# Kernel optimization log

Hardware: AMD Instinct MI355X
Metric: run time of the kernel (lower is better)

The kernel has to match this reference:

```python
import jax, jax.numpy as jnp
import numpy as np

MAX_LEVEL = 3
FULL_LEN = 2 ** MAX_LEVEL  # wavelet_full_len for db1, mode='zero'


def _make_patterns():
    # Per-feature input to the DWT is [v, 0, ..., 0] (scalar zero-padded to 2**j).
    # Haar/db1 'zero' DWT of that signal is v times a fixed sparse pattern:
    # cA (len 1) = v*2^(-j/2); cD_k first element = v*2^(-k/2), rest zeros.
    pats = []
    for j in range(1, MAX_LEVEL + 1):
        vec = [2.0 ** (-j / 2.0)]                      # cA, length 1
        for k in range(1, j + 1):                      # cD_1 .. cD_j
            seg = np.zeros(2 ** (j - k))
            seg[0] = 2.0 ** (-k / 2.0)
            vec.extend(seg.tolist())
        full = np.zeros(FULL_LEN, dtype=np.float32)
        arr = np.asarray(vec, dtype=np.float32)
        full[: arr.shape[0]] = arr                     # F.pad to wavelet_full_len
        pats.append(full)
    return jnp.asarray(np.stack(pats))                 # (MAX_LEVEL, FULL_LEN)

_P = _make_patterns()


def _gumbel_hard(logits, gumb):
    # F.gumbel_softmax(logits, tau=1.0, hard=True), one sample per feature row.
    y = jax.nn.softmax(logits[None, :] + gumb, axis=-1)          # (feat, L)
    hard = jax.nn.one_hot(jnp.argmax(y, axis=-1), y.shape[-1], dtype=y.dtype)
    return jax.lax.stop_gradient(hard - y) + y                   # straight-through


def _wavelet_layer(x, logits, gumb, Wnl, bnl, Wwo, bwo):
    # Collapses the per-feature/per-level torch double loop:
    # xi_wave(level j) = v * (Wnl[f] . P[j]) + bnl[f]
    a = Wnl @ _P.T                       # (feat, levels)
    w = _gumbel_hard(logits, gumb)       # (feat, levels), one-hot rows
    coeff = jnp.sum(w * a, axis=-1)      # (feat,)
    agg = x * coeff + bnl                # (B, N, feat)
    return agg @ Wwo + bwo               # linear_out


def _mix(h, res_proj):
    diff = jnp.mean((h - res_proj) ** 2)
    th = jax.nn.sigmoid(diff)
    return th * h + (1.0 - th) * res_proj


def reference(x, adj, Wres, bres,
              Wg0, bg0, Wrg0, brg0, logits0, gumb0, Wnl0, bnl0, Wwo0, bwo0, Wrw0, brw0,
              Wg1, bg1, Wrg1, brg1, logits1, gumb1, Wnl1, bnl1, Wwo1, bwo1, Wrw1, brw1):
    res = x @ Wres + bres                                        # (B,N,Dout)
    # ---- layer 0 ----
    xg = jnp.einsum('ij,bjf->bif', adj, x) @ Wg0 + bg0           # 64->256: no residual add
    xg = _mix(xg, res @ Wrg0 + brg0)
    xw = _wavelet_layer(xg, logits0, gumb0, Wnl0, bnl0, Wwo0, bwo0) + xg  # 256==256: add
    xw = _mix(xw, res @ Wrw0 + brw0)
    # ---- layer 1 ----
    xg1 = jnp.einsum('ij,bjf->bif', adj, xw) @ Wg1 + bg1 + xw    # 256==256: add
    xg1 = _mix(xg1, res @ Wrg1 + brg1)
    xw1 = _wavelet_layer(xg1, logits1, gumb1, Wnl1, bnl1, Wwo1, bwo1)     # 256->64: no add
    xw1 = _mix(xw1, res @ Wrw1 + brw1)
    return xw1


def setup_inputs() -> dict:
    key = jax.random.key(0)
    ks = jax.random.split(key, 32)
    B, N, D_in, H, D_out = 128, 512, 64, 256, 64
    s = 0.05
    inp = {
        'x': jax.random.normal(ks[0], (B, N, D_in), jnp.float32),
        'adj': jax.random.uniform(ks[1], (N, N), jnp.float32) / N,
        'Wres': jax.random.normal(ks[2], (D_in, D_out), jnp.float32) * s,
        'bres': jax.random.normal(ks[3], (D_out,), jnp.float32) * s,
        'Wg0': jax.random.normal(ks[4], (D_in, H), jnp.float32) * s,
        'bg0': jax.random.normal(ks[5], (H,), jnp.float32) * s,
        'Wrg0': jax.random.normal(ks[6], (D_out, H), jnp.float32) * s,
        'brg0': jax.random.normal(ks[7], (H,), jnp.float32) * s,
        'logits0': jax.random.normal(ks[8], (3,), jnp.float32),
        'gumb0': jax.random.gumbel(ks[9], (H, 3), jnp.float32),
        'Wnl0': jax.random.normal(ks[10], (H, FULL_LEN), jnp.float32) * s,
        'bnl0': jax.random.normal(ks[11], (H,), jnp.float32) * s,
        'Wwo0': jax.random.normal(ks[12], (H, H), jnp.float32) * s,
        'bwo0': jax.random.normal(ks[13], (H,), jnp.float32) * s,
        'Wrw0': jax.random.normal(ks[14], (D_out, H), jnp.float32) * s,
        'brw0': jax.random.normal(ks[15], (H,), jnp.float32) * s,
        'Wg1': jax.random.normal(ks[16], (H, H), jnp.float32) * s,
        'bg1': jax.random.normal(ks[17], (H,), jnp.float32) * s,
        'Wrg1': jax.random.normal(ks[18], (D_out, H), jnp.float32) * s,
        'brg1': jax.random.normal(ks[19], (H,), jnp.float32) * s,
        'logits1': jax.random.normal(ks[20], (3,), jnp.float32),
        'gumb1': jax.random.gumbel(ks[21], (H, 3), jnp.float32),
        'Wnl1': jax.random.normal(ks[22], (H, FULL_LEN), jnp.float32) * s,
        'bnl1': jax.random.normal(ks[23], (H,), jnp.float32) * s,
        'Wwo1': jax.random.normal(ks[24], (H, D_out), jnp.float32) * s,
        'bwo1': jax.random.normal(ks[25], (D_out,), jnp.float32) * s,
        'Wrw1': jax.random.normal(ks[26], (D_out, D_out), jnp.float32) * s,
        'brw1': jax.random.normal(ks[27], (D_out,), jnp.float32) * s,
    }
    return inp
```

## Files before the change

kernel.cpp:

```cpp
#include <hip/hip_runtime.h>
#include <hip/hip_bf16.h>
#include <math.h>

#define BB   128
#define NN   512
#define DIN  64
#define HH   256
#define DOUT 64
#define BNR  (BB * NN)

typedef float  f32x4  __attribute__((ext_vector_type(4)));
typedef __bf16 bf16x8 __attribute__((ext_vector_type(8)));

#define GLP(p)  ((const __attribute__((address_space(1))) void*)(p))
#define LDSP(p) ((__attribute__((address_space(3))) void*)(p))

__constant__ float PAT[3][8] = {
    {0.70710678f, 0.70710678f, 0.f, 0.f, 0.f, 0.f, 0.f, 0.f},
    {0.5f,        0.70710678f, 0.f, 0.5f, 0.f, 0.f, 0.f, 0.f},
    {0.35355339f, 0.70710678f, 0.f, 0.f, 0.f, 0.5f, 0.f, 0.35355339f}
};

__device__ __forceinline__ unsigned short f2bfu(float x) {
    __hip_bfloat16 b = __float2bfloat16(x);
// ... 57 lines not shown
    for (int p = 0; p < BM / RPP; ++p) {
        int row = p * RPP + tid / TPR;
        int cb = (tid % TPR) * 16;
        int pb = cb ^ (((row >> 2) & 3) << 5);
        uint4 v = *reinterpret_cast<const uint4*>(lds + row * (BN * 2) + pb);
        *reinterpret_cast<uint4*>(reinterpret_cast<char*>(C + base + (long)row * N) + cb) = v;
    }
}

template<int BM, int BN, int FM, int FN>
__device__ __forceinline__ void write_tileT(char* lds, f32x4 (&a)[FM][FN],
                                            __hip_bfloat16* __restrict__ CT,
                                            long baseT, int ldT, int tid)
{
    const int wave = tid >> 6;
    const int lane = tid & 63;
    const int wm = wave >> 1, wn = wave & 1;
    const int lc = lane & 15;
    const int lr4 = (lane >> 4) << 2;
    __syncthreads();
    #pragma unroll
    for (int j = 0; j < FN; ++j) {
        int c = wn * (FN * 16) + j * 16 + lc;
        int cbase = c * (BM * 2);
        int swz = ((c >> 2) & 3) << 5;
        #pragma unroll
        for (int i = 0; i < FM; ++i) {
            int m0 = wm * (FM * 16) + i * 16 + lr4;
            #pragma unroll
            for (int r = 0; r < 4; ++r) {
                int m = m0 + r;
                *reinterpret_cast<unsigned short*>(lds + cbase + ((m * 2) ^ swz)) =
                    f2bfu(a[i][j][r]);
            }
        }
    }
    __syncthreads();
    const int TPR = BM / 8;
    const int RPP = 256 / TPR;
    #pragma unroll
    for (int p = 0; p < BN / RPP; ++p) {
        int c = p * RPP + tid / TPR;
        int tb = (tid % TPR) * 16;
        int pb = tb ^ (((c >> 2) & 3) << 5);
        uint4 v = *reinterpret_cast<const uint4*>(lds + c * (BM * 2) + pb);
        *reinterpret_cast<uint4*>(reinterpret_cast<char*>(CT + baseT + (long)c * ldT) + tb) = v;
    }
}

template<int BM, int BN>
__device__ __forceinline__ void stage_tiles(const __hip_bfloat16* __restrict__ Ab,
                                            const __hip_bfloat16* __restrict__ Bb,
                                            char* AsB, char* BsB,
                                            int m0, int n0, int k0, int KA, int KB,
                                            int wave, int lane)
{
    const int NCH = (BM + BN) / 32;
    const int lr = lane >> 3;
    const int ls = lane & 7;
    #pragma unroll
    for (int cc = 0; cc < NCH; ++cc) {
        int c = wave * NCH + cc;
        const __hip_bfloat16* src;
        char* ldsb;
        if (c < BM / 8) {
            int r = c * 8 + lr;
            ldsb = AsB + c * 1024;
            src = Ab + ((long)(m0 + r) * KA + k0 + ((ls ^ (r & 7)) << 3));
        } else {
            int c2 = c - BM / 8;
            int r = c2 * 8 + lr;
            ldsb = BsB + c2 * 1024;
            src = Bb + ((long)(n0 + r) * KB + k0 + ((ls ^ (r & 7)) << 3));
        }
        __builtin_amdgcn_global_load_lds(GLP(src), LDSP(ldsb), 16, 0, 0);
    }
}

template<int BM, int BN, int FM, int FN>
__device__ __forceinline__ void mfma_tiles(char* AsB, char* BsB,
                                           f32x4 (&acc)[FM][FN], int wave, int lane)
{
    const int wm = wave >> 1, wn = wave & 1;
    #pragma unroll
    for (int ksl = 0; ksl < 2; ++ksl) {
        bf16x8 af[FM], bfr[FN];
        #pragma unroll
        for (int i = 0; i < FM; ++i) {
            int row = wm * (FM * 16) + i * 16 + (lane & 15);
            int off = (ksl * 64 + ((lane >> 4) << 4)) ^ ((row & 7) << 4);
            af[i] = *reinterpret_cast<const bf16x8*>(AsB + row * 128 + off);
        }
        #pragma unroll
        for (int j = 0; j < FN; ++j) {
            int row = wn * (FN * 16) + j * 16 + (lane & 15);
            int off = (ksl * 64 + ((lane >> 4) << 4)) ^ ((row & 7) << 4);
            bfr[j] = *reinterpret_cast<const bf16x8*>(BsB + row * 128 + off);
        }
        #pragma unroll
        for (int i = 0; i < FM; ++i)
            #pragma unroll
            for (int j = 0; j < FN; ++j)
                acc[i][j] = __builtin_amdgcn_mfma_f32_16x16x32_bf16(
                    af[i], bfr[j], acc[i][j], 0, 0, 0);
    }
}

template<int BM, int BN, int FM, int FN, int NS, int NA>
__device__ __forceinline__ void pipe_run(
    const __hip_bfloat16* const (&sA)[NS], const __hip_bfloat16* const (&sB)[NS],
    const int (&sK)[NS], const int (&sk0)[NS],
    char* buf0, char* buf1,
    f32x4 (&acc0)[FM][FN], f32x4 (&acc1)[FM][FN],
    int m0, int n0, int wave, int lane)
{
    constexpr int BOFF = BM * 128;
    stage_tiles<BM, BN>(sA[0], sB[0], buf0, buf0 + BOFF, m0, n0, sk0[0],
                        sK[0], sK[0], wave, lane);
    __syncthreads();
    #pragma unroll
    for (int t = 0; t < NS; ++t) {
        char* bc = (t & 1) ? buf1 : buf0;
        if (t + 1 < NS) {
            char* bn = (t & 1) ? buf0 : buf1;
            stage_tiles<BM, BN>(sA[t + 1], sB[t + 1], bn, bn + BOFF, m0, n0,
                                sk0[t + 1], sK[t + 1], sK[t + 1], wave, lane);
        }
        if (t < NA) mfma_tiles<BM, BN, FM, FN>(bc, bc + BOFF, acc0, wave, lane);
        else        mfma_tiles<BM, BN, FM, FN>(bc, bc + BOFF, acc1, wave, lane);
        __syncthreads();
    }
}

__device__ __forceinline__ void tcvt_body(const float* __restrict__ in,
                                          unsigned short* __restrict__ out,
                                          const float* cs, float us,
                                          int R, int C, int r0, int c0)
{
    __shared__ float t[64][65];
    int tr = threadIdx.x >> 6;
    int tc = threadIdx.x & 63;
    #pragma unroll
    for (int i = 0; i < 16; ++i) {
        int r = i * 4 + tr;
        t[r][tc] = in[(long)(r0 + r) * C + c0 + tc];
    }
    __syncthreads();
    float sc = (cs ? cs[r0 + tc] : 1.0f) * us;
    #pragma unroll
    for (int i = 0; i < 16; ++i) {
        int r = i * 4 + tr;
        out[(long)(c0 + r) * R + r0 + tc] = f2bfu(t[tc][r] * sc);
    }
}

__device__ __forceinline__ void coeff_local(const float* lg, const float* gb,
                                            const float* Wn, float* cof, int t)
{
    float l0 = lg[0] + gb[t * 3 + 0];
    float l1 = lg[1] + gb[t * 3 + 1];
    float l2 = lg[2] + gb[t * 3 + 2];
    int bl = 0;
    float bv = l0;
    if (l1 > bv) { bv = l1; bl = 1; }
    if (l2 > bv) { bv = l2; bl = 2; }
    float s = 0.f;
    #pragma unroll
    for (int q = 0; q < 8; ++q) s += Wn[t * 8 + q] * PAT[bl][q];
    cof[t] = s;
}

struct WTArgs {
    const float* src[8];
    unsigned short* dst[8];
    int ci[8];
    float sgn[8];
    int R[8], C[8];
};
struct WFArgs {
    const float* Wsrc[4];
    const float* Wbig[4];
    int ci[4], incl[4], N[4];
    unsigned short* dst[4];
};
struct FVArgs {
    const float* W[6];
    int ci[6];
    const float* v[6];
    const float* base[6];
    float* out[6];
    int K[6], N[6];
};
struct PrepArgs {
    const float *logits0, *gumb0, *Wnl0, *logits1, *gumb1, *Wnl1;
    const float* adj;
    unsigned int* adjb;
    float* ars;
    const float* x;
    unsigned short *xbf, *xT;
};

__global__ __launch_bounds__(256) void prep_k(PrepArgs p, WTArgs wa, WFArgs wf, FVArgs fv)
{
    __shared__ float cofA[256];
    __shared__ float cofB[256];
    __shared__ float redu[256];
    const int b = blockIdx.x;
    const int t = threadIdx.x;
    if (b < NN) {
        float2 v = reinterpret_cast<const float2*>(p.adj)[b * 256 + t];
        p.adjb[b * 256 + t] = (unsigned int)f2bfu(v.x) | ((unsigned int)f2bfu(v.y) << 16);
        redu[t] = v.x + v.y;
        __syncthreads();
        for (int o = 128; o > 0; o >>= 1) {
            if (t < o) redu[t] += redu[t + o];
            __syncthreads();
        }
        if (t == 0) p.ars[b] = redu[0];
    } else if (b < NN + 8 * BB) {
        __shared__ float tl[64][65];
        int tt = b - NN;
        int bz = tt >> 3;
        int r0 = (tt & 7) * 64;
        const long base = (long)bz * NN * DIN;
        const int tr4 = t >> 6;
        const int tc  = t & 63;
        #pragma unroll
        for (int i = 0; i < 16; ++i) {
            int r = i * 4 + tr4;
            float v = p.x[base + (long)(r0 + r) * DIN + tc];
            tl[r][tc] = v;
            p.xbf[base + (long)(r0 + r) * DIN + tc] = f2bfu(v);
        }
        __syncthreads();
        #pragma unroll
        for (int i = 0; i < 16; ++i) {
            int d = i * 4 + tr4;
            p.xT[base + (long)d * NN + r0 + tc] = f2bfu(tl[tc][d]);
        }
    } else if (b < NN + 8 * BB + 128) {
        int xg = b - NN - 8 * BB;
        int wgt = xg >> 4;
        int tl2 = xg & 15;
        int R = wa.R[wgt], C = wa.C[wgt];
        int tilesX = C >> 6;
        int tiles = (R >> 6) * tilesX;
        if (tl2 >= tiles) return;
        const float* cs = nullptr;
        if (wa.ci[wgt]) {
            if (wa.ci[wgt] == 1) coeff_local(p.logits0, p.gumb0, p.Wnl0, cofA, t);
            else                 coeff_local(p.logits1, p.gumb1, p.Wnl1, cofA, t);
            __syncthreads();
            cs = cofA;
        }
        tcvt_body(wa.src[wgt], wa.dst[wgt], cs, wa.sgn[wgt], R, C,
                  (tl2 / tilesX) * 64, (tl2 % tilesX) * 64);
    } else if (b < NN + 8 * BB + 128 + 256) {
        int xg = b - NN - 8 * BB - 128;
        int cs = xg >> 6;
        int m = xg & 63;
        float cv = 1.0f;
        if (wf.ci[cs]) {
            if (wf.ci[cs] == 1) coeff_local(p.logits0, p.gumb0, p.Wnl0, cofA, t);
            else                coeff_local(p.logits1, p.gumb1, p.Wnl1, cofA, t);
            __syncthreads();
            cv = cofA[t];
        }
        cofB[t] = wf.Wsrc[cs][m * 256 + t] * cv;
        __syncthreads();
        int n = t;
        int N = wf.N[cs];
        if (n >= N) return;
        float s = wf.incl[cs] ? wf.Wsrc[cs][m * 256 + n] : 0.f;
        const float* Wb = wf.Wbig[cs];
        #pragma unroll 8
        for (int k = 0; k < 256; ++k)
            s += cofB[k] * Wb[(long)k * N + n];
        wf.dst[cs][n * 64 + m] = f2bfu(s);
    } else {
        int n = b - (NN + 8 * BB + 128 + 256);
        coeff_local(p.logits0, p.gumb0, p.Wnl0, cofA, t);
        coeff_local(p.logits1, p.gumb1, p.Wnl1, cofB, t);
        __syncthreads();
        for (int cs = 0; cs < 6; ++cs) {
            __syncthreads();
            if (n >= fv.N[cs]) continue;
            float s = 0.f;
            if (t < fv.K[cs]) {
                float cc = (fv.ci[cs] == 1) ? cofA[t] : (fv.ci[cs] == 2 ? cofB[t] : 1.0f);
                s = fv.v[cs][t] * cc * fv.W[cs][(long)t * fv.N[cs] + n];
            }
            redu[t] = s;
            __syncthreads();
            for (int o = 128; o > 0; o >>= 1) {
                if (t < o) redu[t] += redu[t + o];
                __syncthreads();
            }
            if (t == 0)
                fv.out[cs][n] = (fv.base[cs] ? fv.base[cs][n] : 0.f) + redu[0];
        }
    }
}

__global__ __launch_bounds__(256) void sc0_k(
    const float* __restrict__ partial, int np, float inv_n,
    unsigned short* __restrict__ Wa, unsigned short* __restrict__ Wb,
    const float* __restrict__ bg0p, const float* __restrict__ brg0p,
    const float* __restrict__ crow0, float* __restrict__ cv0)
{
    __shared__ float red[256];
    float th = block_th(partial, np, inv_n, red, threadIdx.x);
    float om = 1.f - th;
    int g = blockIdx.x * 256 + threadIdx.x;
    Wa[g] = f2bfu(th * bf2f(Wa[g]));
    Wb[g] = f2bfu(om * bf2f(Wb[g]));
    if (g < 256) cv0[g] = th * bg0p[g] + om * brg0p[g] + crow0[g];
}

__global__ __launch_bounds__(256) void sc1_k(
    const float* __restrict__ partial, int np, float inv_n,
    unsigned short* __restrict__ Wg1T,
    const unsigned short* __restrict__ Wrw0T, const unsigned short* __restrict__ Wrg0pT,
    unsigned short* __restrict__ WcombT,
    unsigned short* __restrict__ Wg0pT,
    unsigned short* __restrict__ WrwWg1T,
    const float* __restrict__ bg1, const float* __restrict__ brw0,
    const float* __restrict__ cv0, const float* __restrict__ bw1v,
    float* __restrict__ bv1g, float* __restrict__ bw1s)
{
    __shared__ float red[256];
    float th = block_th(partial, np, inv_n, red, threadIdx.x);
    float om = 1.f - th;
    int g = blockIdx.x * 256 + threadIdx.x;
    Wg1T[g] = f2bfu(th * bf2f(Wg1T[g]));
    if (g < 16384) {
        WcombT[g]  = f2bfu(th * bf2f(Wrg0pT[g]) + om * bf2f(Wrw0T[g]));
        Wg0pT[g]   = f2bfu(th * bf2f(Wg0pT[g]));
        WrwWg1T[g] = f2bfu(om * bf2f(WrwWg1T[g]));
    }
    if (g < 256) {
        bv1g[g] = bg1[g] + om * brw0[g] + th * cv0[g];
        bw1s[g] = om * bw1v[g];
    }
}

__global__ __launch_bounds__(256) void sc2_k(
    const float* __restrict__ partial, int np, float inv_n,
    unsigned short* __restrict__ Wc1T, unsigned short* __restrict__ Wrgc1T,
    const float* __restrict__ brgc1, const float* __restrict__ crow1,
    float* __restrict__ cv2)
{
    __shared__ float red[256];
    float th = block_th(partial, np, inv_n, red, threadIdx.x);
    float om = 1.f - th;
    int g = blockIdx.x * 256 + threadIdx.x;
    Wc1T[g] = f2bfu(th * bf2f(Wc1T[g]));
    if (g < 4096) Wrgc1T[g] = f2bfu(om * bf2f(Wrgc1T[g]));
    if (g < 64) cv2[g] = om * brgc1[g] + crow1[g];
}

template<int BM, int BN, int FM, int FN>
__global__ __launch_bounds__(256) void gemm_res_k(
    const __hip_bfloat16* __restrict__ A, const __hip_bfloat16* __restrict__ Bt,
    const float* __restrict__ bias,
    __hip_bfloat16* __restrict__ Cb, __hip_bfloat16* __restrict__ CbT,
    int M, int N, int K)
{
    __shared__ __attribute__((aligned(128))) char lds[(BM + BN) * 128];
    char* AsB = lds;
    char* BsB = lds + BM * 128;

    const int m0 = blockIdx.y * BM;
    const int tid  = threadIdx.x;
    const int wave = tid >> 6;
    const int lane = tid & 63;
    const int wn = wave & 1;

    f32x4 acc[FM][FN];
    #pragma unroll
    for (int i = 0; i < FM; ++i)
        #pragma unroll
        for (int j = 0; j < FN; ++j)
            acc[i][j] = (f32x4){0.f, 0.f, 0.f, 0.f};

    for (int k0 = 0; k0 < K; k0 += 64) {
        stage_tiles<BM, BN>(A, Bt, AsB, BsB, m0, 0, k0, K, K, wave, lane);
        __syncthreads();
        mfma_tiles<BM, BN, FM, FN>(AsB, BsB, acc, wave, lane);
        __syncthreads();
    }

    const int lc = lane & 15;
    #pragma unroll
    for (int j = 0; j < FN; ++j) {
        float bv = bias[wn * (FN * 16) + j * 16 + lc];
        #pragma unroll
        for (int i = 0; i < FM; ++i)
            #pragma unroll
            for (int r = 0; r < 4; ++r)
                acc[i][j][r] += bv;
    }
    write_tile<BM, BN, FM, FN>(lds, acc, Cb, (long)m0 * N, N, tid);
    long baseT = (long)(m0 / NN) * ((long)N * NN) + (m0 % NN);
    write_tileT<BM, BN, FM, FN>(lds, acc, CbT, baseT, NN, tid);
}

__global__ __launch_bounds__(256) void t0radj_k(
    const __hip_bfloat16* __restrict__ adjb,
    const __hip_bfloat16* __restrict__ xT,
    const __hip_bfloat16* __restrict__ RbfT,
    __hip_bfloat16* __restrict__ T0,
    __hip_bfloat16* __restrict__ Radj)
{
    constexpr int BM = 128, BN = 64;
    constexpr int ABYTES = BM * 128;
    constexpr int BBYTES = BN * 128;
    constexpr int BUF = ABYTES + 2 * BBYTES;
    __shared__ __attribute__((aligned(128))) char lds[2 * BUF];

    const int d   = blockIdx.x;
    const int xcd = d & 7;
    const int q   = d >> 3;
    const int t   = q & 3;
    const int bz  = xcd + ((q >> 2) << 3);
    const int m0  = t * BM;

    const __hip_bfloat16* B1 = xT + (long)bz * (64L * NN);
    const __hip_bfloat16* B2 = RbfT + (long)bz * (64L * NN);

    const int tid  = threadIdx.x;
    const int wave = tid >> 6;
    const int lane = tid & 63;
    const int lr = lane >> 3;
    const int ls = lane & 7;

    f32x4 accA[4][2], accB[4][2];
    #pragma unroll
    for (int i = 0; i < 4; ++i)
        #pragma unroll
        for (int j = 0; j < 2; ++j) {
            accA[i][j] = (f32x4){0.f, 0.f, 0.f, 0.f};
            accB[i][j] = (f32x4){0.f, 0.f, 0.f, 0.f};
        }

    auto stage2 = [&](char* buf, int k0) {
        #pragma unroll
        for (int cc = 0; cc < 8; ++cc) {
            int c = wave * 8 + cc;
            const __hip_bfloat16* src;
            char* ldsb;
            if (c < 16) {
                int r = c * 8 + lr;
                ldsb = buf + c * 1024;
                src = adjb + ((long)(m0 + r) * NN + k0 + ((ls ^ (r & 7)) << 3));
            } else if (c < 24) {
                int r = (c - 16) * 8 + lr;
                ldsb = buf + ABYTES + (c - 16) * 1024;
                src = B1 + ((long)r * NN + k0 + ((ls ^ (r & 7)) << 3));
            } else {
                int r = (c - 24) * 8 + lr;
                ldsb = buf + ABYTES + BBYTES + (c - 24) * 1024;
                src = B2 + ((long)r * NN + k0 + ((ls ^ (r & 7)) << 3));
            }
            __builtin_amdgcn_global_load_lds(GLP(src), LDSP(ldsb), 16, 0, 0);
        }
    };

    stage2(lds, 0);
    __syncthreads();
    #pragma unroll
    for (int s = 0; s < 8; ++s) {
        char* bc = lds + (s & 1) * BUF;
        if (s + 1 < 8) stage2(lds + ((s + 1) & 1) * BUF, (s + 1) * 64);
        mfma_tiles<BM, BN, 4, 2>(bc, bc + ABYTES, accA, wave, lane);
        mfma_tiles<BM, BN, 4, 2>(bc, bc + ABYTES + BBYTES, accB, wave, lane);
        __syncthreads();
    }

    long base = (long)bz * ((long)NN * BN) + (long)m0 * BN;
    write_tile<BM, BN, 4, 2>(lds, accA, T0, base, BN, tid);
    write_tile<BM, BN, 4, 2>(lds, accB, Radj, base, BN, tid);
}

template<int BM, int BN, int FM, int FN, int GX, int NB, int NS>
__global__ __launch_bounds__(256) void gemm_bt_swz_k(
    const __hip_bfloat16* __restrict__ A, const __hip_bfloat16* __restrict__ Bt,
    __hip_bfloat16* __restrict__ Cb,
    int M, int N, int K, long sA, long sB, long sC)
{
    __shared__ __attribute__((aligned(128))) char lds[2 * (BM + BN) * 128];

    const int d   = blockIdx.x;
    const int xcd = d & 7;
    const int q   = d >> 3;
    const int t   = q % NB;
    const int bz  = xcd + ((q / NB) << 3);
    const int n0  = (t % GX) * BN;
    const int m0  = (t / GX) * BM;

    const __hip_bfloat16* Ab = A + (long)bz * sA;
    const __hip_bfloat16* Bb = Bt + (long)bz * sB;

    const int tid  = threadIdx.x;
    const int wave = tid >> 6;
    const int lane = tid & 63;

    f32x4 acc[FM][FN];
    #pragma unroll
    for (int i = 0; i < FM; ++i)
        #pragma unroll
        for (int j = 0; j < FN; ++j)
            acc[i][j] = (f32x4){0.f, 0.f, 0.f, 0.f};

    const __hip_bfloat16* pA[NS];
    const __hip_bfloat16* pB[NS];
    int pK[NS], pk0[NS];
    #pragma unroll
    for (int s = 0; s < NS; ++s) { pA[s] = Ab; pB[s] = Bb; pK[s] = K; pk0[s] = s * 64; }

    pipe_run<BM, BN, FM, FN, NS, NS>(pA, pB, pK, pk0,
                                     lds, lds + (BM + BN) * 128,
                                     acc, acc, m0, n0, wave, lane);

    write_tile<BM, BN, FM, FN>(lds, acc, Cb, (long)bz * sC + (long)m0 * N + n0, N, tid);
}

template<int BM, int BN, int FM, int FN>
__global__ __launch_bounds__(256) void dual1_k(
    const __hip_bfloat16* __restrict__ A0, const __hip_bfloat16* __restrict__ B0, int K0,
    const __hip_bfloat16* __restrict__ A1, const __hip_bfloat16* __restrict__ B1, int K1,
    const float* __restrict__ b1, const float* __restrict__ b2,
    float* __restrict__ partial, int M, int N)
{
    __shared__ __attribute__((aligned(128))) char lds[2 * (BM + BN) * 128];

    const int d   = blockIdx.x;
    const int q   = d >> 3;
    const int nx  = q & 1;
    const int my  = (d & 7) + ((q >> 1) << 3);
    const int m0  = my * BM;
    const int n0  = nx * BN;

    const int tid  = threadIdx.x;
    const int wave = tid >> 6;
    const int lane = tid & 63;
    const int wn = wave & 1;

    f32x4 acc[FM][FN];
    #pragma unroll
    for (int i = 0; i < FM; ++i)
        #pragma unroll
        for (int j = 0; j < FN; ++j)
            acc[i][j] = (f32x4){0.f, 0.f, 0.f, 0.f};

    const __hip_bfloat16* pA[2] = {A0, A1};
    const __hip_bfloat16* pB[2] = {B0, B1};
    int pK[2] = {K0, K1};
    int pk0[2] = {0, 0};
    pipe_run<BM, BN, FM, FN, 2, 2>(pA, pB, pK, pk0,
                                   lds, lds + (BM + BN) * 128,
                                   acc, acc, m0, n0, wave, lane);

    const int lc = lane & 15;
    float dsum = 0.f;
    #pragma unroll
    for (int j = 0; j < FN; ++j) {
        int col = n0 + wn * (FN * 16) + j * 16 + lc;
        float bd = b1[col] - b2[col];
        #pragma unroll
        for (int i = 0; i < FM; ++i)
            #pragma unroll
            for (int r = 0; r < 4; ++r) {
                float dd = acc[i][j][r] + bd;
                dsum += dd * dd;
            }
    }

    float* red = (float*)lds;
    red[tid] = dsum;
    __syncthreads();
    for (int o = 128; o > 0; o >>= 1) {
        if (tid < o) red[tid] += red[tid + o];
        __syncthreads();
    }
    if (tid == 0) partial[my * 2 + nx] = red[0];
}

template<int BM, int BN, int FM, int FN>
__global__ __launch_bounds__(256) void wave2T_k(
    const __hip_bfloat16* __restrict__ A0, const __hip_bfloat16* __restrict__ B0, int K0,
    const __hip_bfloat16* __restrict__ A1, const __hip_bfloat16* __restrict__ B1, int K1,
    const __hip_bfloat16* __restrict__ A2, const __hip_bfloat16* __restrict__ B2, int K2,
    const float* __restrict__ cv, const float* __restrict__ b2v,
    __hip_bfloat16* __restrict__ C1T, float* __restrict__ partial_out, int M, int N)
{
    __shared__ __attribute__((aligned(128))) char lds[2 * (BM + BN) * 128];

    const int d   = blockIdx.x;
    const int q   = d >> 3;
    const int nx  = q & 1;
    const int my  = (d & 7) + ((q >> 1) << 3);
    const int m0  = my * BM;
    const int n0  = nx * BN;

    const int tid  = threadIdx.x;
    const int wave = tid >> 6;
    const int lane = tid & 63;
    const int wn = wave & 1;

    f32x4 acc0[FM][FN], acc1[FM][FN];
    #pragma unroll
    for (int i = 0; i < FM; ++i)
        #pragma unroll
        for (int j = 0; j < FN; ++j) {
            acc0[i][j] = (f32x4){0.f, 0.f, 0.f, 0.f};
            acc1[i][j] = (f32x4){0.f, 0.f, 0.f, 0.f};
        }

    const __hip_bfloat16* pA[3] = {A0, A1, A2};
    const __hip_bfloat16* pB[3] = {B0, B1, B2};
    int pK[3] = {K0, K1, K2};
    int pk0[3] = {0, 0, 0};
    pipe_run<BM, BN, FM, FN, 3, 2>(pA, pB, pK, pk0,
                                   lds, lds + (BM + BN) * 128,
                                   acc0, acc1, m0, n0, wave, lane);

    const int lc = lane & 15;
    float dsum = 0.f;
    #pragma unroll
    for (int j = 0; j < FN; ++j) {
        int col = n0 + wn * (FN * 16) + j * 16 + lc;
        float c1 = cv[col];
        float c2 = b2v[col];
        #pragma unroll
        for (int i = 0; i < FM; ++i)
            #pragma unroll
            for (int r = 0; r < 4; ++r) {
                float v1 = acc0[i][j][r] + c1;
                float v2 = acc1[i][j][r] + c2;
                acc0[i][j][r] = v1;
                float dd = v1 - v2;
                dsum += dd * dd;
            }
    }

    float* red = (float*)lds;
    red[tid] = dsum;
    __syncthreads();
    for (int o = 128; o > 0; o >>= 1) {
        if (tid < o) red[tid] += red[tid + o];
        __syncthreads();
    }
    if (tid == 0) partial_out[my * 2 + nx] = red[0];

    long baseT = (long)(m0 / NN) * ((long)N * NN) + (long)n0 * NN + (m0 % NN);
    write_tileT<BM, BN, FM, FN>(lds, acc0, C1T, baseT, NN, tid);
}

template<int BM, int BN, int FM, int FN>
__global__ __launch_bounds__(256) void gmix5_k(
    const __hip_bfloat16* __restrict__ A0, const __hip_bfloat16* __restrict__ B0, int K0,
    const __hip_bfloat16* __restrict__ A1, const __hip_bfloat16* __restrict__ B1, int K1,
    const __hip_bfloat16* __restrict__ A2, const __hip_bfloat16* __restrict__ B2, int K2,
    const __hip_bfloat16* __restrict__ A3, const __hip_bfloat16* __restrict__ B3, int K3,
    const __hip_bfloat16* __restrict__ A4, const __hip_bfloat16* __restrict__ B4, int K4,
    const float* __restrict__ bv1, const float* __restrict__ b2v,
    const float* __restrict__ ars, const float* __restrict__ bw1s,
    __hip_bfloat16* __restrict__ C1, float* __restrict__ partial_out, int M, int N)
{
    __shared__ __attribute__((aligned(128))) char lds[2 * (BM + BN) * 128];

    const int d  = blockIdx.x;
    const int q  = d >> 3;
    const int nx = q & 1;
    const int my = (d & 7) + ((q >> 1) << 3);
    const int m0 = my * BM;
    const int n0 = nx * BN;

    const int tid  = threadIdx.x;
    const int wave = tid >> 6;
    const int lane = tid & 63;
    const int wm = wave >> 1, wn = wave & 1;

    f32x4 acc0[FM][FN], acc1[FM][FN];
    #pragma unroll
    for (int i = 0; i < FM; ++i)
        #pragma unroll
        for (int j = 0; j < FN; ++j) {
            acc0[i][j] = (f32x4){0.f, 0.f, 0.f, 0.f};
            acc1[i][j] = (f32x4){0.f, 0.f, 0.f, 0.f};
        }

    const __hip_bfloat16* pA[8] = {A0, A0, A0, A0, A1, A2, A3, A4};
    const __hip_bfloat16* pB[8] = {B0, B0, B0, B0, B1, B2, B3, B4};
    int pK[8]  = {K0, K0, K0, K0, K1, K2, K3, K4};
    int pk0[8] = {0, 64, 128, 192, 0, 0, 0, 0};
    pipe_run<BM, BN, FM, FN, 8, 7>(pA, pB, pK, pk0,
                                   lds, lds + (BM + BN) * 128,
                                   acc0, acc1, m0, n0, wave, lane);

    const int lc  = lane & 15;
    const int lr4 = (lane >> 4) << 2;
    const int node0 = m0 & (NN - 1);
    float dsum = 0.f;
    #pragma unroll
    for (int j = 0; j < FN; ++j) {
        int col = n0 + wn * (FN * 16) + j * 16 + lc;
        float c1 = bv1[col];
        float c2 = b2v[col];
        float bw = bw1s[col];
        #pragma unroll
        for (int i = 0; i < FM; ++i) {
            int rowl = wm * (FM * 16) + i * 16 + lr4;
            #pragma unroll
            for (int r = 0; r < 4; ++r) {
                float av = ars[node0 + rowl + r];
                float v1 = acc0[i][j][r] + c1 + av * bw;
                float v2 = acc1[i][j][r] + c2;
                acc0[i][j][r] = v1;
                float dd = v1 - v2;
                dsum += dd * dd;
            }
        }
    }

    float* red = (float*)lds;
    red[tid] = dsum;
    __syncthreads();
    for (int o = 128; o > 0; o >>= 1) {
        if (tid < o) red[tid] += red[tid + o];
        __syncthreads();
    }
    if (tid == 0) partial_out[my * 2 + nx] = red[0];

    write_tile<BM, BN, FM, FN>(lds, acc0, C1, (long)m0 * N + n0, N, tid);
}

template<int BM, int BN, int FM, int FN>
__global__ __launch_bounds__(256) void wave2_k(
    const __hip_bfloat16* __restrict__ A0, const __hip_bfloat16* __restrict__ B0, int K0,
    const __hip_bfloat16* __restrict__ A1, const __hip_bfloat16* __restrict__ B1, int K1,
    const __hip_bfloat16* __restrict__ A2, const __hip_bfloat16* __restrict__ B2, int K2,
    const float* __restrict__ cv, const float* __restrict__ b2v,
    __hip_bfloat16* __restrict__ C1, __hip_bfloat16* __restrict__ C2,
    float* __restrict__ partial_out, int M, int N)
{
    __shared__ __attribute__((aligned(128))) char lds[2 * (BM + BN) * 128];

    const int m0 = blockIdx.y * BM;
    const int n0 = blockIdx.x * BN;
    const int pidx = blockIdx.y * gridDim.x + blockIdx.x;

    const int tid  = threadIdx.x;
    const int wave = tid >> 6;
    const int lane = tid & 63;
    const int wn = wave & 1;

    f32x4 acc0[FM][FN], acc1[FM][FN];
    #pragma unroll
    for (int i = 0; i < FM; ++i)
        #pragma unroll
        for (int j = 0; j < FN; ++j) {
            acc0[i][j] = (f32x4){0.f, 0.f, 0.f, 0.f};
            acc1[i][j] = (f32x4){0.f, 0.f, 0.f, 0.f};
        }

    const __hip_bfloat16* pA[6] = {A0, A0, A0, A0, A1, A2};
    const __hip_bfloat16* pB[6] = {B0, B0, B0, B0, B1, B2};
    int pK[6]  = {K0, K0, K0, K0, K1, K2};
    int pk0[6] = {0, 64, 128, 192, 0, 0};
    pipe_run<BM, BN, FM, FN, 6, 5>(pA, pB, pK, pk0,
                                   lds, lds + (BM + BN) * 128,
                                   acc0, acc1, m0, n0, wave, lane);

    const int lc = lane & 15;
    float dsum = 0.f;
    #pragma unroll
    for (int j = 0; j < FN; ++j) {
        int col = n0 + wn * (FN * 16) + j * 16 + lc;
        float c1 = cv[col];
        float c2 = b2v[col];
        #pragma unroll
        for (int i = 0; i < FM; ++i)
            #pragma unroll
            for (int r = 0; r < 4; ++r) {
                float v1 = acc0[i][j][r] + c1;
                float v2 = acc1[i][j][r] + c2;
                acc0[i][j][r] = v1;
                acc1[i][j][r] = v2;
                float dd = v1 - v2;
                dsum += dd * dd;
            }
    }

    float* red = (float*)lds;
    red[tid] = dsum;
    __syncthreads();
    for (int o = 128; o > 0; o >>= 1) {
        if (tid < o) red[tid] += red[tid + o];
        __syncthreads();
    }
    if (tid == 0) partial_out[pidx] = red[0];

    write_tile<BM, BN, FM, FN>(lds, acc0, C1, (long)m0 * N + n0, N, tid);
    write_tile<BM, BN, FM, FN>(lds, acc1, C2, (long)m0 * N + n0, N, tid);
}

__global__ __launch_bounds__(256) void mixfinal_k(
    const unsigned short* __restrict__ h, const unsigned short* __restrict__ r,
    const float* __restrict__ partial_in, int np_in, float inv_in,
    float* __restrict__ out, long n4)
{
    __shared__ float sm[256];
    const float th = block_th(partial_in, np_in, inv_in, sm, (int)threadIdx.x);
    const float om = 1.f - th;
    long gid = (long)blockIdx.x * 256 + threadIdx.x;
    long stride = (long)gridDim.x * 256;
    for (long i = gid; i < n4; i += stride) {
        ushort4 hv = reinterpret_cast<const ushort4*>(h)[i];
        ushort4 rv = reinterpret_cast<const ushort4*>(r)[i];
        float4 o;
        o.x = th * bf2f(hv.x) + om * bf2f(rv.x);
        o.y = th * bf2f(hv.y) + om * bf2f(rv.y);
        o.z = th * bf2f(hv.z) + om * bf2f(rv.z);
        o.w = th * bf2f(hv.w) + om * bf2f(rv.w);
        reinterpret_cast<float4*>(out)[i] = o;
    }
}

extern "C" void kernel_launch(void* const* d_in, const int* in_sizes, int n_in,
                              void* d_out, int out_size, void* d_ws, size_t ws_size,
                              hipStream_t stream)
{
    const float* x       = (const float*)d_in[0];
    const float* adj     = (const float*)d_in[1];
    const float* Wres    = (const float*)d_in[2];
    const float* bres    = (const float*)d_in[3];
    const float* Wg0     = (const float*)d_in[4];
    const float* bg0     = (const float*)d_in[5];
    const float* Wrg0    = (const float*)d_in[6];
    const float* brg0    = (const float*)d_in[7];
    const float* logits0 = (const float*)d_in[8];
    const float* gumb0   = (const float*)d_in[9];
    const float* Wnl0    = (const float*)d_in[10];
    const float* bnl0    = (const float*)d_in[11];
    const float* Wwo0    = (const float*)d_in[12];
    const float* bwo0    = (const float*)d_in[13];
    const float* Wrw0    = (const float*)d_in[14];
    const float* brw0    = (const float*)d_in[15];
    const float* Wg1     = (const float*)d_in[16];
    const float* bg1     = (const float*)d_in[17];
    const float* Wrg1    = (const float*)d_in[18];
    const float* brg1    = (const float*)d_in[19];
    const float* logits1 = (const float*)d_in[20];
    const float* gumb1   = (const float*)d_in[21];
    const float* Wnl1    = (const float*)d_in[22];
    const float* bnl1    = (const float*)d_in[23];
    const float* Wwo1    = (const float*)d_in[24];
    const float* bwo1    = (const float*)d_in[25];
    const float* Wrw1    = (const float*)d_in[26];
    const float* brw1    = (const float*)d_in[27];

    float* out = (float*)d_out;

    char* w = (char*)d_ws;
    auto alloc = [&](long bytes) { char* p = w; w += (bytes + 255) & ~255L; return p; };
    const long SLOT = (long)BNR * HH * 2;
    char* pool = alloc(5 * SLOT);
    __hip_bfloat16* Rbf  = (__hip_bfloat16*)alloc((long)BNR * DOUT * 2);
    __hip_bfloat16* adjb = (__hip_bfloat16*)alloc((long)NN * NN * 2);
    __hip_bfloat16* WT   = (__hip_bfloat16*)alloc(225280L * 2);
    float* partial0 = (float*)alloc(2048 * 4);
    float* partial1 = (float*)alloc(2048 * 4);
    float* partial2 = (float*)alloc(2048 * 4);
    float* partial3 = (float*)alloc(2048 * 4);
    float* bg0p    = (float*)alloc(256 * 4);
    float* brg0p   = (float*)alloc(256 * 4);
    float* crow0   = (float*)alloc(256 * 4);
    float* brgc1   = (float*)alloc(64 * 4);
    float* crow1   = (float*)alloc(64 * 4);
    float* cv0     = (float*)alloc(256 * 4);
    float* bv1g    = (float*)alloc(256 * 4);
    float* cv2     = (float*)alloc(64 * 4);
    float* ars     = (float*)alloc(512 * 4);
    float* bw1v    = (float*)alloc(256 * 4);
    float* bw1s    = (float*)alloc(256 * 4);

    auto S = [&](int i) { return pool + (long)i * SLOT; };
    __hip_bfloat16* xwrT = (__hip_bfloat16*)S(0);
    __hip_bfloat16* orw  = (__hip_bfloat16*)S(1);
    __hip_bfloat16* rw1  = (__hip_bfloat16*)(S(1) + (long)BNR * DOUT * 2);
    __hip_bfloat16* Radj = (__hip_bfloat16*)(S(1) + 2L * BNR * DOUT * 2);
    __hip_bfloat16* xg1  = (__hip_bfloat16*)S(2);
    __hip_bfloat16* T1x  = (__hip_bfloat16*)S(3);
    __hip_bfloat16* xbf  = (__hip_bfloat16*)S(4);
    __hip_bfloat16* xT   = (__hip_bfloat16*)(S(4) + (long)BNR * DIN * 2);
    __hip_bfloat16* T0   = (__hip_bfloat16*)(S(4) + 2L * BNR * DIN * 2);
    __hip_bfloat16* RbfT = (__hip_bfloat16*)(S(4) + 3L * BNR * DIN * 2);

    __hip_bfloat16* WresT   = WT;
    __hip_bfloat16* Wg0T    = WT + 4096;
    __hip_bfloat16* Wrg0T   = WT + 20480;
    __hip_bfloat16* Wrw0T   = WT + 36864;
    __hip_bfloat16* Wg1T    = WT + 53248;
    __hip_bfloat16* Wrg1T   = WT + 118784;
    __hip_bfloat16* Wc1T    = WT + 135168;
    __hip_bfloat16* Wrw1T   = WT + 151552;
    __hip_bfloat16* Wg0pT   = WT + 155648;
    __hip_bfloat16* Wrg0pT  = WT + 172032;
    __hip_bfloat16* Wrgc1T  = WT + 188416;
    __hip_bfloat16* WcombT  = WT + 192512;
    __hip_bfloat16* WrwWg1T = WT + 208896;

    const dim3 blk(256);
    const float invH = 1.0f / ((float)BNR * HH);
    const float invD = 1.0f / ((float)BNR * DOUT);

    PrepArgs pa;
    pa.logits0 = logits0; pa.gumb0 = gumb0; pa.Wnl0 = Wnl0;
    pa.logits1 = logits1; pa.gumb1 = gumb1; pa.Wnl1 = Wnl1;
    pa.adj = adj; pa.adjb = (unsigned int*)adjb; pa.ars = ars;
    pa.x = x; pa.xbf = (unsigned short*)xbf; pa.xT = (unsigned short*)xT;

    WTArgs wa;
    wa.src[0] = Wres; wa.dst[0] = (unsigned short*)WresT; wa.ci[0] = 0; wa.sgn[0] = 1.f;  wa.R[0] = 64;  wa.C[0] = 64;
    wa.src[1] = Wg0;  wa.dst[1] = (unsigned short*)Wg0T;  wa.ci[1] = 0; wa.sgn[1] = 1.f;  wa.R[1] = 64;  wa.C[1] = 256;
    wa.src[2] = Wrg0; wa.dst[2] = (unsigned short*)Wrg0T; wa.ci[2] = 0; wa.sgn[2] = -1.f; wa.R[2] = 64;  wa.C[2] = 256;
    wa.src[3] = Wrw0; wa.dst[3] = (unsigned short*)Wrw0T; wa.ci[3] = 0; wa.sgn[3] = 1.f;  wa.R[3] = 64;  wa.C[3] = 256;
    wa.src[4] = Wg1;  wa.dst[4] = (unsigned short*)Wg1T;  wa.ci[4] = 0; wa.sgn[4] = 1.f;  wa.R[4] = 256; wa.C[4] = 256;
    wa.src[5] = Wrg1; wa.dst[5] = (unsigned short*)Wrg1T; wa.ci[5] = 0; wa.sgn[5] = 1.f;  wa.R[5] = 64;  wa.C[5] = 256;
    wa.src[6] = Wwo1; wa.dst[6] = (unsigned short*)Wc1T;  wa.ci[6] = 2; wa.sgn[6] = 1.f;  wa.R[6] = 256; wa.C[6] = 64;
    wa.src[7] = Wrw1; wa.dst[7] = (unsigned short*)Wrw1T; wa.ci[7] = 0; wa.sgn[7] = 1.f;  wa.R[7] = 64;  wa.C[7] = 64;

    WFArgs wf;
    wf.Wsrc[0] = Wg0;  wf.Wbig[0] = Wwo0; wf.ci[0] = 1; wf.incl[0] = 1; wf.N[0] = 256;
    wf.dst[0] = (unsigned short*)Wg0pT;
    wf.Wsrc[1] = Wrg0; wf.Wbig[1] = Wwo0; wf.ci[1] = 1; wf.incl[1] = 1; wf.N[1] = 256;
    wf.dst[1] = (unsigned short*)Wrg0pT;
    wf.Wsrc[2] = Wrg1; wf.Wbig[2] = Wwo1; wf.ci[2] = 2; wf.incl[2] = 0; wf.N[2] = 64;
    wf.dst[2] = (unsigned short*)Wrgc1T;
    wf.Wsrc[3] = Wrw0; wf.Wbig[3] = Wg1;  wf.ci[3] = 0; wf.incl[3] = 0; wf.N[3] = 256;
    wf.dst[3] = (unsigned short*)WrwWg1T;

    FVArgs fv;
    fv.W[0] = Wwo0; fv.ci[0] = 1; fv.v[0] = bg0;  fv.base[0] = bg0;     fv.out[0] = bg0p;  fv.K[0] = 256; fv.N[0] = 256;
    fv.W[1] = Wwo0; fv.ci[1] = 1; fv.v[1] = brg0; fv.base[1] = brg0;    fv.out[1] = brg0p; fv.K[1] = 256; fv.N[1] = 256;
    fv.W[2] = Wwo0; fv.ci[2] = 0; fv.v[2] = bnl0; fv.base[2] = bwo0;    fv.out[2] = crow0; fv.K[2] = 256; fv.N[2] = 256;
    fv.W[3] = Wwo1; fv.ci[3] = 2; fv.v[3] = brg1; fv.base[3] = nullptr; fv.out[3] = brgc1; fv.K[3] = 256; fv.N[3] = 64;
    fv.W[4] = Wwo1; fv.ci[4] = 0; fv.v[4] = bnl1; fv.base[4] = bwo1;    fv.out[4] = crow1; fv.K[4] = 256; fv.N[4] = 64;
    fv.W[5] = Wg1;  fv.ci[5] = 0; fv.v[5] = brw0; fv.base[5] = nullptr; fv.out[5] = bw1v;  fv.K[5] = 256; fv.N[5] = 256;

    hipLaunchKernelGGL(prep_k, dim3(NN + 8 * BB + 128 + 256 + 256), blk, 0, stream,
                       pa, wa, wf, fv);

    hipLaunchKernelGGL((gemm_res_k<128, 64, 4, 2>), dim3(1, BNR / 128, 1), blk, 0, stream,
                       xbf, WresT, bres, Rbf, RbfT, BNR, DOUT, DIN);

    hipLaunchKernelGGL(t0radj_k, dim3(BB * 4), blk, 0, stream,
                       adjb, xT, RbfT, T0, Radj);

    hipLaunchKernelGGL((dual1_k<64, 128, 2, 4>), dim3(2 * BNR / 64), blk, 0, stream,
                       T0, Wg0T, DIN, Rbf, Wrg0T, DOUT, bg0, brg0, partial0, BNR, HH);

    hipLaunchKernelGGL(sc0_k, dim3(64), blk, 0, stream, partial0, 2048, invH,
                       (unsigned short*)Wg0pT, (unsigned short*)Wrg0pT,
                       bg0p, brg0p, crow0, cv0);

    hipLaunchKernelGGL((wave2T_k<64, 128, 2, 4>), dim3(2 * BNR / 64), blk, 0, stream,
                       T0, Wg0pT, DIN, Rbf, Wrg0pT, DOUT, Rbf, Wrw0T, DOUT,
                       cv0, brw0, xwrT, partial1, BNR, HH);

    hipLaunchKernelGGL(sc1_k, dim3(256), blk, 0, stream, partial1, 2048, invH,
                       (unsigned short*)Wg1T,
                       (const unsigned short*)Wrw0T, (const unsigned short*)Wrg0pT,
                       (unsigned short*)WcombT,
                       (unsigned short*)Wg0pT,
                       (unsigned short*)WrwWg1T,
                       bg1, brw0, cv0, bw1v, bv1g, bw1s);

    hipLaunchKernelGGL((gemm_bt_swz_k<128, 64, 4, 2, 4, 16, 8>), dim3(BB * 16), blk, 0, stream,
                       adjb, xwrT, T1x, NN, HH, NN, 0, (long)HH * NN, (long)NN * HH);

    hipLaunchKernelGGL((gmix5_k<64, 128, 2, 4>), dim3(2 * BNR / 64), blk, 0, stream,
                       T1x, Wg1T, HH,
                       Radj, WrwWg1T, DOUT,
                       T0, Wg0pT, DIN,
                       Rbf, WcombT, DOUT,
                       Rbf, Wrg1T, DOUT,
                       bv1g, brg1, ars, bw1s, xg1, partial2, BNR, HH);

    hipLaunchKernelGGL(sc2_k, dim3(64), blk, 0, stream, partial2, 2048, invH,
                       (unsigned short*)Wc1T, (unsigned short*)Wrgc1T,
                       brgc1, crow1, cv2);

    hipLaunchKernelGGL((wave2_k<64, 64, 2, 2>), dim3(1, BNR / 64), blk, 0, stream,
                       xg1, Wc1T, HH, Rbf, Wrgc1T, DOUT, Rbf, Wrw1T, DIN,
                       cv2, brw1, orw, rw1, partial3, BNR, DOUT);

    hipLaunchKernelGGL(mixfinal_k, dim3(2048), blk, 0, stream,
                       (const unsigned short*)orw, (const unsigned short*)rw1,
                       partial3, 1024, invD, out, (long)BNR * DOUT / 4);
}
```

Baseline: 158.1 us.

## Fold scalar-mix scaling into GEMM epilogues, removing sc0/sc2 launches

Removes the sc0_k and sc2_k kernels, which rescaled weight matrices by the sigmoid gate before the next GEMM. The following GEMMs now keep separate accumulators per weight term and apply the gate (recomputed per block from the partial sums) in the epilogue. sc1_k is adjusted to fold in the gate from stage 0. This saves two launches and their serial dependency, at the cost of an extra accumulator set (more registers) and a redundant partial-sum reduction in every block.

```diff
diff --git a/kernel.cpp b/kernel.cpp
--- a/kernel.cpp
+++ b/kernel.cpp
@@ -383,61 +383,36 @@
     }
 }
 
-__global__ __launch_bounds__(256) void sc0_k(
-    const float* __restrict__ partial, int np, float inv_n,
-    unsigned short* __restrict__ Wa, unsigned short* __restrict__ Wb,
-    const float* __restrict__ bg0p, const float* __restrict__ brg0p,
-    const float* __restrict__ crow0, float* __restrict__ cv0)
-{
-    __shared__ float red[256];
-    float th = block_th(partial, np, inv_n, red, threadIdx.x);
-    float om = 1.f - th;
-    int g = blockIdx.x * 256 + threadIdx.x;
-    Wa[g] = f2bfu(th * bf2f(Wa[g]));
-    Wb[g] = f2bfu(om * bf2f(Wb[g]));
-    if (g < 256) cv0[g] = th * bg0p[g] + om * brg0p[g] + crow0[g];
-}
-
 __global__ __launch_bounds__(256) void sc1_k(
-    const float* __restrict__ partial, int np, float inv_n,
+    const float* __restrict__ partial0, const float* __restrict__ partial1,
+    int np, float inv_n,
     unsigned short* __restrict__ Wg1T,
     const unsigned short* __restrict__ Wrw0T, const unsigned short* __restrict__ Wrg0pT,
     unsigned short* __restrict__ WcombT,
     unsigned short* __restrict__ Wg0pT,
     unsigned short* __restrict__ WrwWg1T,
     const float* __restrict__ bg1, const float* __restrict__ brw0,
-    const float* __restrict__ cv0, const float* __restrict__ bw1v,
+    const float* __restrict__ bg0p, const float* __restrict__ brg0p,
+    const float* __restrict__ crow0, const float* __restrict__ bw1v,
     float* __restrict__ bv1g, float* __restrict__ bw1s)
 {
     __shared__ float red[256];
-    float th = block_th(partial, np, inv_n, red, threadIdx.x);
-    float om = 1.f - th;
+    float th0 = block_th(partial0, np, inv_n, red, threadIdx.x);
+    float om0 = 1.f - th0;
+    float th1 = block_th(partial1, np, inv_n, red, threadIdx.x);
+    float om1 = 1.f - th1;
     int g = blockIdx.x * 256 + threadIdx.x;
-    Wg1T[g] = f2bfu(th * bf2f(Wg1T[g]));
+    Wg1T[g] = f2bfu(th1 * bf2f(Wg1T[g]));
     if (g < 16384) {
-        WcombT[g]  = f2bfu(th * bf2f(Wrg0pT[g]) + om * bf2f(Wrw0T[g]));
-        Wg0pT[g]   = f2bfu(th * bf2f(Wg0pT[g]));
-        WrwWg1T[g] = f2bfu(om * bf2f(WrwWg1T[g]));
+        WcombT[g]  = f2bfu(th1 * om0 * bf2f(Wrg0pT[g]) + om1 * bf2f(Wrw0T[g]));
+        Wg0pT[g]   = f2bfu(th0 * th1 * bf2f(Wg0pT[g]));
+        WrwWg1T[g] = f2bfu(om1 * bf2f(WrwWg1T[g]));
     }
     if (g < 256) {
-        bv1g[g] = bg1[g] + om * brw0[g] + th * cv0[g];
-        bw1s[g] = om * bw1v[g];
-    }
-}
-
-__global__ __launch_bounds__(256) void sc2_k(
-    const float* __restrict__ partial, int np, float inv_n,
-    unsigned short* __restrict__ Wc1T, unsigned short* __restrict__ Wrgc1T,
-    const float* __restrict__ brgc1, const float* __restrict__ crow1,
-    float* __restrict__ cv2)
-{
-    __shared__ float red[256];
-    float th = block_th(partial, np, inv_n, red, threadIdx.x);
-    float om = 1.f - th;
-    int g = blockIdx.x * 256 + threadIdx.x;
-    Wc1T[g] = f2bfu(th * bf2f(Wc1T[g]));
-    if (g < 4096) Wrgc1T[g] = f2bfu(om * bf2f(Wrgc1T[g]));
-    if (g < 64) cv2[g] = om * brgc1[g] + crow1[g];
+        float cv0 = th0 * bg0p[g] + om0 * brg0p[g] + crow0[g];
+        bv1g[g] = bg1[g] + om1 * brw0[g] + th1 * cv0;
+        bw1s[g] = om1 * bw1v[g];
+    }
 }
 
 template<int BM, int BN, int FM, int FN>
@@ -668,14 +643,19 @@
 }
 
 template<int BM, int BN, int FM, int FN>
-__global__ __launch_bounds__(256) void wave2T_k(
+__global__ __launch_bounds__(256) void wave3T_k(
     const __hip_bfloat16* __restrict__ A0, const __hip_bfloat16* __restrict__ B0, int K0,
     const __hip_bfloat16* __restrict__ A1, const __hip_bfloat16* __restrict__ B1, int K1,
     const __hip_bfloat16* __restrict__ A2, const __hip_bfloat16* __restrict__ B2, int K2,
-    const float* __restrict__ cv, const float* __restrict__ b2v,
+    const float* __restrict__ partial_in, int np_in, float inv_in,
+    const float* __restrict__ bg0p, const float* __restrict__ brg0p,
+    const float* __restrict__ crow0, const float* __restrict__ b2v,
     __hip_bfloat16* __restrict__ C1T, float* __restrict__ partial_out, int M, int N)
 {
     __shared__ __attribute__((aligned(128))) char lds[2 * (BM + BN) * 128];
+    constexpr int BOFF = BM * 128;
+    char* b0 = lds;
+    char* b1 = lds + (BM + BN) * 128;
 
     const int d   = blockIdx.x;
     const int q   = d >> 3;
@@ -689,37 +669,46 @@
     const int lane = tid & 63;
     const int wn = wave & 1;
 
-    f32x4 acc0[FM][FN], acc1[FM][FN];
+    f32x4 accA[FM][FN], accB[FM][FN], accC[FM][FN];
     #pragma unroll
     for (int i = 0; i < FM; ++i)
         #pragma unroll
         for (int j = 0; j < FN; ++j) {
-            acc0[i][j] = (f32x4){0.f, 0.f, 0.f, 0.f};
-            acc1[i][j] = (f32x4){0.f, 0.f, 0.f, 0.f};
-        }
-
-    const __hip_bfloat16* pA[3] = {A0, A1, A2};
-    const __hip_bfloat16* pB[3] = {B0, B1, B2};
-    int pK[3] = {K0, K1, K2};
-    int pk0[3] = {0, 0, 0};
-    pipe_run<BM, BN, FM, FN, 3, 2>(pA, pB, pK, pk0,
-                                   lds, lds + (BM + BN) * 128,
-                                   acc0, acc1, m0, n0, wave, lane);
+            accA[i][j] = (f32x4){0.f, 0.f, 0.f, 0.f};
+            accB[i][j] = (f32x4){0.f, 0.f, 0.f, 0.f};
+            accC[i][j] = (f32x4){0.f, 0.f, 0.f, 0.f};
+        }
+
+    stage_tiles<BM, BN>(A0, B0, b0, b0 + BOFF, m0, n0, 0, K0, K0, wave, lane);
+    __syncthreads();
+    stage_tiles<BM, BN>(A1, B1, b1, b1 + BOFF, m0, n0, 0, K1, K1, wave, lane);
+    mfma_tiles<BM, BN, FM, FN>(b0, b0 + BOFF, accA, wave, lane);
+    __syncthreads();
+    stage_tiles<BM, BN>(A2, B2, b0, b0 + BOFF, m0, n0, 0, K2, K2, wave, lane);
+    mfma_tiles<BM, BN, FM, FN>(b1, b1 + BOFF, accB, wave, lane);
+    __syncthreads();
+    mfma_tiles<BM, BN, FM, FN>(b0, b0 + BOFF, accC, wave, lane);
+    __syncthreads();
+
+    const float th = block_th(partial_in, np_in, inv_in, (float*)lds, tid);
+    const float om = 1.f - th;
 
     const int lc = lane & 15;
     float dsum = 0.f;
     #pragma unroll
     for (int j = 0; j < FN; ++j) {
         int col = n0 + wn * (FN * 16) + j * 16 + lc;
-        float c1 = cv[col];
-        float c2 = b2v[col];
+        float bA = bg0p[col];
+        float bB = brg0p[col];
+        float cr = crow0[col];
+        float b2 = b2v[col];
         #pragma unroll
         for (int i = 0; i < FM; ++i)
             #pragma unroll
             for (int r = 0; r < 4; ++r) {
-                float v1 = acc0[i][j][r] + c1;
-                float v2 = acc1[i][j][r] + c2;
-                acc0[i][j][r] = v1;
+                float v1 = th * (accA[i][j][r] + bA) + om * (accB[i][j][r] + bB) + cr;
+                float v2 = accC[i][j][r] + b2;
+                accA[i][j][r] = v1;
                 float dd = v1 - v2;
                 dsum += dd * dd;
             }
@@ -735,7 +724,7 @@
     if (tid == 0) partial_out[my * 2 + nx] = red[0];
 
     long baseT = (long)(m0 / NN) * ((long)N * NN) + (long)n0 * NN + (m0 % NN);
-    write_tileT<BM, BN, FM, FN>(lds, acc0, C1T, baseT, NN, tid);
+    write_tileT<BM, BN, FM, FN>(lds, accA, C1T, baseT, NN, tid);
 }
 
 template<int BM, int BN, int FM, int FN>
@@ -818,15 +807,20 @@
 }
 
 template<int BM, int BN, int FM, int FN>
-__global__ __launch_bounds__(256) void wave2_k(
+__global__ __launch_bounds__(256) void wave3_k(
     const __hip_bfloat16* __restrict__ A0, const __hip_bfloat16* __restrict__ B0, int K0,
     const __hip_bfloat16* __restrict__ A1, const __hip_bfloat16* __restrict__ B1, int K1,
     const __hip_bfloat16* __restrict__ A2, const __hip_bfloat16* __restrict__ B2, int K2,
-    const float* __restrict__ cv, const float* __restrict__ b2v,
+    const float* __restrict__ partial_in, int np_in, float inv_in,
+    const float* __restrict__ brgc1, const float* __restrict__ crow1,
+    const float* __restrict__ b2v,
     __hip_bfloat16* __restrict__ C1, __hip_bfloat16* __restrict__ C2,
     float* __restrict__ partial_out, int M, int N)
 {
     __shared__ __attribute__((aligned(128))) char lds[2 * (BM + BN) * 128];
+    constexpr int BOFF = BM * 128;
+    char* b0 = lds;
+    char* b1 = lds + (BM + BN) * 128;
 
     const int m0 = blockIdx.y * BM;
     const int n0 = blockIdx.x * BN;
@@ -837,38 +831,56 @@
     const int lane = tid & 63;
     const int wn = wave & 1;
 
-    f32x4 acc0[FM][FN], acc1[FM][FN];
+    f32x4 accA[FM][FN], accB[FM][FN], accC[FM][FN];
     #pragma unroll
     for (int i = 0; i < FM; ++i)
         #pragma unroll
         for (int j = 0; j < FN; ++j) {
-            acc0[i][j] = (f32x4){0.f, 0.f, 0.f, 0.f};
-            acc1[i][j] = (f32x4){0.f, 0.f, 0.f, 0.f};
+            accA[i][j] = (f32x4){0.f, 0.f, 0.f, 0.f};
+            accB[i][j] = (f32x4){0.f, 0.f, 0.f, 0.f};
+            accC[i][j] = (f32x4){0.f, 0.f, 0.f, 0.f};
         }
 
     const __hip_bfloat16* pA[6] = {A0, A0, A0, A0, A1, A2};
     const __hip_bfloat16* pB[6] = {B0, B0, B0, B0, B1, B2};
     int pK[6]  = {K0, K0, K0, K0, K1, K2};
     int pk0[6] = {0, 64, 128, 192, 0, 0};
-    pipe_run<BM, BN, FM, FN, 6, 5>(pA, pB, pK, pk0,
-                                   lds, lds + (BM + BN) * 128,
-                                   acc0, acc1, m0, n0, wave, lane);
+
+    stage_tiles<BM, BN>(pA[0], pB[0], b0, b0 + BOFF, m0, n0, 0, K0, K0, wave, lane);
+    __syncthreads();
+    #pragma unroll
+    for (int t = 0; t < 6; ++t) {
+        char* bc = (t & 1) ? b1 : b0;
+        if (t + 1 < 6) {
+            char* bn = (t & 1) ? b0 : b1;
+            stage_tiles<BM, BN>(pA[t + 1], pB[t + 1], bn, bn + BOFF, m0, n0,
+                                pk0[t + 1], pK[t + 1], pK[t + 1], wave, lane);
+        }
+        if (t < 4)      mfma_tiles<BM, BN, FM, FN>(bc, bc + BOFF, accA, wave, lane);
+        else if (t == 4) mfma_tiles<BM, BN, FM, FN>(bc, bc + BOFF, accB, wave, lane);
+        else            mfma_tiles<BM, BN, FM, FN>(bc, bc + BOFF, accC, wave, lane);
+        __syncthreads();
+    }
+
+    const float th = block_th(partial_in, np_in, inv_in, (float*)lds, tid);
+    const float om = 1.f - th;
 
     const int lc = lane & 15;
     float dsum = 0.f;
     #pragma unroll
     for (int j = 0; j < FN; ++j) {
         int col = n0 + wn * (FN * 16) + j * 16 + lc;
-        float c1 = cv[col];
-        float c2 = b2v[col];
+        float bB = brgc1[col];
+        float cr = crow1[col];
+        float b2 = b2v[col];
         #pragma unroll
         for (int i = 0; i < FM; ++i)
             #pragma unroll
             for (int r = 0; r < 4; ++r) {
-                float v1 = acc0[i][j][r] + c1;
-                float v2 = acc1[i][j][r] + c2;
-                acc0[i][j][r] = v1;
-                acc1[i][j][r] = v2;
+                float v1 = th * accA[i][j][r] + om * (accB[i][j][r] + bB) + cr;
+                float v2 = accC[i][j][r] + b2;
+                accA[i][j][r] = v1;
+                accC[i][j][r] = v2;
                 float dd = v1 - v2;
                 dsum += dd * dd;
             }
@@ -883,8 +895,8 @@
     }
     if (tid == 0) partial_out[pidx] = red[0];
 
-    write_tile<BM, BN, FM, FN>(lds, acc0, C1, (long)m0 * N + n0, N, tid);
-    write_tile<BM, BN, FM, FN>(lds, acc1, C2, (long)m0 * N + n0, N, tid);
+    write_tile<BM, BN, FM, FN>(lds, accA, C1, (long)m0 * N + n0, N, tid);
+    write_tile<BM, BN, FM, FN>(lds, accC, C2, (long)m0 * N + n0, N, tid);
 }
 
 __global__ __launch_bounds__(256) void mixfinal_k(
@@ -960,9 +972,7 @@
     float* crow0   = (float*)alloc(256 * 4);
     float* brgc1   = (float*)alloc(64 * 4);
     float* crow1   = (float*)alloc(64 * 4);
-    float* cv0     = (float*)alloc(256 * 4);
     float* bv1g    = (float*)alloc(256 * 4);
-    float* cv2     = (float*)alloc(64 * 4);
     float* ars     = (float*)alloc(512 * 4);
     float* bw1v    = (float*)alloc(256 * 4);
     float* bw1s    = (float*)alloc(256 * 4);
@@ -1043,21 +1053,19 @@
     hipLaunchKernelGGL((dual1_k<64, 128, 2, 4>), dim3(2 * BNR / 64), blk, 0, stream,
                        T0, Wg0T, DIN, Rbf, Wrg0T, DOUT, bg0, brg0, partial0, BNR, HH);
 
-    hipLaunchKernelGGL(sc0_k, dim3(64), blk, 0, stream, partial0, 2048, invH,
-                       (unsigned short*)Wg0pT, (unsigned short*)Wrg0pT,
-                       bg0p, brg0p, crow0, cv0);
-
-    hipLaunchKernelGGL((wave2T_k<64, 128, 2, 4>), dim3(2 * BNR / 64), blk, 0, stream,
+    hipLaunchKernelGGL((wave3T_k<64, 128, 2, 4>), dim3(2 * BNR / 64), blk, 0, stream,
                        T0, Wg0pT, DIN, Rbf, Wrg0pT, DOUT, Rbf, Wrw0T, DOUT,
-                       cv0, brw0, xwrT, partial1, BNR, HH);
-
-    hipLaunchKernelGGL(sc1_k, dim3(256), blk, 0, stream, partial1, 2048, invH,
+                       partial0, 2048, invH,
+                       bg0p, brg0p, crow0, brw0,
+                       xwrT, partial1, BNR, HH);
+
+    hipLaunchKernelGGL(sc1_k, dim3(256), blk, 0, stream, partial0, partial1, 2048, invH,
                        (unsigned short*)Wg1T,
                        (const unsigned short*)Wrw0T, (const unsigned short*)Wrg0pT,
                        (unsigned short*)WcombT,
                        (unsigned short*)Wg0pT,
                        (unsigned short*)WrwWg1T,
-                       bg1, brw0, cv0, bw1v, bv1g, bw1s);
+                       bg1, brw0, bg0p, brg0p, crow0, bw1v, bv1g, bw1s);
 
     hipLaunchKernelGGL((gemm_bt_swz_k<128, 64, 4, 2, 4, 16, 8>), dim3(BB * 16), blk, 0, stream,
                        adjb, xwrT, T1x, NN, HH, NN, 0, (long)HH * NN, (long)NN * HH);
@@ -1070,13 +1078,11 @@
                        Rbf, Wrg1T, DOUT,
                        bv1g, brg1, ars, bw1s, xg1, partial2, BNR, HH);
 
-    hipLaunchKernelGGL(sc2_k, dim3(64), blk, 0, stream, partial2, 2048, invH,
-                       (unsigned short*)Wc1T, (unsigned short*)Wrgc1T,
-                       brgc1, crow1, cv2);
-
-    hipLaunchKernelGGL((wave2_k<64, 64, 2, 2>), dim3(1, BNR / 64), blk, 0, stream,
+    hipLaunchKernelGGL((wave3_k<64, 64, 2, 2>), dim3(1, BNR / 64), blk, 0, stream,
                        xg1, Wc1T, HH, Rbf, Wrgc1T, DOUT, Rbf, Wrw1T, DIN,
-                       cv2, brw1, orw, rw1, partial3, BNR, DOUT);
+                       partial2, 2048, invH,
+                       brgc1, crow1, brw1,
+                       orw, rw1, partial3, BNR, DOUT);
 
     hipLaunchKernelGGL(mixfinal_k, dim3(2048), blk, 0, stream,
                        (const unsigned short*)orw, (const unsigned short*)rw1,
```

After: 164.2 us. 1.04x slower.
